# Optimization experiments

Measured on AMD Instinct MI355X. Metric: run time of the kernel, lower is better.

The kernel has to match this reference:

```python
import jax, jax.numpy as jnp
import numpy as np

HIDDEN_DIM = 512  # global scale divisor used in the original layer


def setup_inputs() -> dict:
    key = jax.random.key(0)
    k1, k2 = jax.random.split(key)
    B, S, H = 32, 8192, 512
    states_h = jax.random.normal(k1, (B, H), dtype=jnp.float32)
    enc_out = jax.random.normal(k2, (B, S, H), dtype=jnp.float32)
    return {"states_h": states_h, "enc_out": enc_out}


def reference(states_h, enc_out):
    # align_score = matmul(enc_out, dec_h^T) / hidden_dim -> [B, S, 1]
    align = jnp.einsum("bsh,bh->bs", enc_out, states_h) / HIDDEN_DIM
    # softmax over the sequence axis (axis=1 in the original [B,S,1] tensor)
    weights = jax.nn.softmax(align, axis=1)[:, :, None]           # [B, S, 1]
    # context = sum_s enc_out * weights -> [B, H], then expand to [B, 1, H]
    context = jnp.einsum("bsh,bs->bh", enc_out, weights[:, :, 0])
    context = context[:, None, :]                                  # [B, 1, H]
    return (context, weights)
```

## Files before the change

kernel.cpp:

```cpp
#include <hip/hip_runtime.h>
#include <hip/hip_bf16.h>
#include <math.h>


#define BB 32
#define SS 8192
#define HH 512
#define NB 32
#define WPB 4
#define NP (NB * WPB)
#define RPW (SS / NP)

__global__ __launch_bounds__(256, 4) void attn_pass1(
    const float* __restrict__ states, const float* __restrict__ enc,
    float* __restrict__ align, float* __restrict__ pm,
    float* __restrict__ pl, float* __restrict__ pC)
{
    const int b     = blockIdx.x >> 5;
    const int chunk = blockIdx.x & (NB - 1);
    const int lane  = threadIdx.x & 63;
    const int wv    = threadIdx.x >> 6;
    const int p     = chunk * WPB + wv;

    const float4* st = (const float4*)(states + (size_t)b * HH);
    const float4 sh0 = st[lane];
    const float4 sh1 = st[lane + 64];

    const float* rowbase = enc + ((size_t)b * SS + (size_t)p * RPW) * HH;

    float  m = -1e30f, l = 0.0f;
    float4 c0 = make_float4(0.f, 0.f, 0.f, 0.f);
    float4 c1 = make_float4(0.f, 0.f, 0.f, 0.f);
    float  my_a = 0.0f;

    #pragma unroll 4
    for (int r = 0; r < RPW; ++r) {
        const float4* rp = (const float4*)(rowbase + (size_t)r * HH);
        float4 e0 = rp[lane];
        float4 e1 = rp[lane + 64];

        float d = e0.x*sh0.x + e0.y*sh0.y + e0.z*sh0.z + e0.w*sh0.w
                + e1.x*sh1.x + e1.y*sh1.y + e1.z*sh1.z + e1.w*sh1.w;
        #pragma unroll
        for (int off = 1; off < 64; off <<= 1)
            d += __shfl_xor(d, off, 64);

        float a = d * (1.0f / 512.0f);
        my_a = (r == lane) ? a : my_a;

        float mn    = fmaxf(m, a);
        float scale = __expf(m - mn);
        float pr    = __expf(a - mn);
        l = fmaf(l, scale, pr);
        c0.x = fmaf(pr, e0.x, c0.x * scale);
        c0.y = fmaf(pr, e0.y, c0.y * scale);
        c0.z = fmaf(pr, e0.z, c0.z * scale);
        c0.w = fmaf(pr, e0.w, c0.w * scale);
        c1.x = fmaf(pr, e1.x, c1.x * scale);
        c1.y = fmaf(pr, e1.y, c1.y * scale);
        c1.z = fmaf(pr, e1.z, c1.z * scale);
        c1.w = fmaf(pr, e1.w, c1.w * scale);
        m = mn;
    }

    align[(size_t)b * SS + (size_t)p * RPW + lane] = my_a;
    if (lane == 0) {
        pm[b * NP + p] = m;
        pl[b * NP + p] = l;
    }
    float4* Cp = (float4*)(pC + (size_t)(b * NP + p) * HH);
    Cp[lane]      = c0;
    Cp[lane + 64] = c1;
}

__global__ __launch_bounds__(256) void attn_pass2(
    const float* __restrict__ align, const float* __restrict__ pm,
    const float* __restrict__ pl, const float* __restrict__ pC,
    float* __restrict__ out_ctx, float* __restrict__ out_w)
{
    const int b = blockIdx.x;
    const int t = threadIdx.x;

    __shared__ float red[NP];
    __shared__ float s_w[NP];
    __shared__ float s_M, s_invL;

    if (t < NP) red[t] = pm[b * NP + t];
    __syncthreads();
    if (t == 0) {
        float M = -1e30f;
        for (int i = 0; i < NP; ++i) M = fmaxf(M, red[i]);
        s_M = M;
    }
    __syncthreads();
    const float M = s_M;
    if (t < NP) s_w[t] = __expf(red[t] - M);
    __syncthreads();
    if (t == 0) {
        float L = 0.0f;
        for (int i = 0; i < NP; ++i) L += s_w[i] * pl[b * NP + i];
        s_invL = 1.0f / L;
    }
    __syncthreads();
    const float invL = s_invL;

    float acc0 = 0.0f, acc1 = 0.0f;
    const float* Cb = pC + (size_t)b * NP * HH;
    #pragma unroll 4
    for (int p = 0; p < NP; ++p) {
        float w = s_w[p];
        acc0 = fmaf(w, Cb[(size_t)p * HH + t], acc0);
        acc1 = fmaf(w, Cb[(size_t)p * HH + t + 256], acc1);
    }
    out_ctx[b * HH + t]       = acc0 * invL;
    out_ctx[b * HH + t + 256] = acc1 * invL;

    const float* al = align + (size_t)b * SS;
    float*       ow = out_w + (size_t)b * SS;
    for (int s = t; s < SS; s += 256)
        ow[s] = __expf(al[s] - M) * invL;
}

extern "C" void kernel_launch(void* const* d_in, const int* in_sizes, int n_in,
                              void* d_out, int out_size, void* d_ws, size_t ws_size,
                              hipStream_t stream) {
    const float* states = (const float*)d_in[0];
    const float* enc    = (const float*)d_in[1];

    float* out_ctx = (float*)d_out;
    float* out_w   = (float*)d_out + (size_t)BB * HH;

    float* ws_align = (float*)d_ws;
    float* ws_pm    = ws_align + (size_t)BB * SS;
    float* ws_pl    = ws_pm    + (size_t)BB * NP;
    float* ws_pC    = ws_pl    + (size_t)BB * NP;

    attn_pass1<<<BB * NB, 256, 0, stream>>>(states, enc, ws_align, ws_pm, ws_pl, ws_pC);
    attn_pass2<<<BB, 256, 0, stream>>>(ws_align, ws_pm, ws_pl, ws_pC, out_ctx, out_w);
}
```

Measured before the change: 684.4 us.

## Double the pass-1 split, prefetch rows, and parallelise pass-2 reduction across blocks

Pass 1 now uses 64 blocks per batch row, so each wave handles 32 rows instead of 64, and occupancy is raised to 6. Each wave software-prefetches encoder rows two iterations ahead. The online softmax update is made branchy on a wave-uniform score so that only one exp is computed per row. Pass 2 is split into 8 blocks per batch, with shuffle-based max/sum reductions, float4 accumulation of the partial contexts, and vectorised weight writes. The trade-off is doubling the partial-context workspace traffic and extra register pressure from the prefetch buffers.

```diff
diff --git a/kernel.cpp b/kernel.cpp
--- a/kernel.cpp
+++ b/kernel.cpp
@@ -6,17 +6,18 @@
 #define BB 32
 #define SS 8192
 #define HH 512
-#define NB 32
+#define NB 64
 #define WPB 4
 #define NP (NB * WPB)
 #define RPW (SS / NP)
+#define WCH 8
 
-__global__ __launch_bounds__(256, 4) void attn_pass1(
+__global__ __launch_bounds__(256, 6) void attn_pass1(
     const float* __restrict__ states, const float* __restrict__ enc,
     float* __restrict__ align, float* __restrict__ pm,
     float* __restrict__ pl, float* __restrict__ pC)
 {
-    const int b     = blockIdx.x >> 5;
+    const int b     = blockIdx.x >> 6;
     const int chunk = blockIdx.x & (NB - 1);
     const int lane  = threadIdx.x & 63;
     const int wv    = threadIdx.x >> 6;
@@ -26,18 +27,22 @@
     const float4 sh0 = st[lane];
     const float4 sh1 = st[lane + 64];
 
-    const float* rowbase = enc + ((size_t)b * SS + (size_t)p * RPW) * HH;
+    const float4* rp = (const float4*)(enc + ((size_t)b * SS + (size_t)p * RPW) * HH);
 
     float  m = -1e30f, l = 0.0f;
     float4 c0 = make_float4(0.f, 0.f, 0.f, 0.f);
     float4 c1 = make_float4(0.f, 0.f, 0.f, 0.f);
     float  my_a = 0.0f;
 
+    float4 e0 = rp[lane],        e1 = rp[lane + 64];
+    float4 f0 = rp[128 + lane],  f1 = rp[128 + lane + 64];
+
     #pragma unroll 4
     for (int r = 0; r < RPW; ++r) {
-        const float4* rp = (const float4*)(rowbase + (size_t)r * HH);
-        float4 e0 = rp[lane];
-        float4 e1 = rp[lane + 64];
+        const int rn = (r + 2 < RPW) ? (r + 2) : (RPW - 1);
+        const float4* q = rp + (size_t)rn * 128;
+        float4 g0 = q[lane];
+        float4 g1 = q[lane + 64];
 
         float d = e0.x*sh0.x + e0.y*sh0.y + e0.z*sh0.z + e0.w*sh0.w
                 + e1.x*sh1.x + e1.y*sh1.y + e1.z*sh1.z + e1.w*sh1.w;
@@ -46,24 +51,41 @@
             d += __shfl_xor(d, off, 64);
 
         float a = d * (1.0f / 512.0f);
+        a = __uint_as_float(__builtin_amdgcn_readfirstlane(__float_as_uint(a)));
+
         my_a = (r == lane) ? a : my_a;
 
-        float mn    = fmaxf(m, a);
-        float scale = __expf(m - mn);
-        float pr    = __expf(a - mn);
-        l = fmaf(l, scale, pr);
-        c0.x = fmaf(pr, e0.x, c0.x * scale);
-        c0.y = fmaf(pr, e0.y, c0.y * scale);
-        c0.z = fmaf(pr, e0.z, c0.z * scale);
-        c0.w = fmaf(pr, e0.w, c0.w * scale);
-        c1.x = fmaf(pr, e1.x, c1.x * scale);
-        c1.y = fmaf(pr, e1.y, c1.y * scale);
-        c1.z = fmaf(pr, e1.z, c1.z * scale);
-        c1.w = fmaf(pr, e1.w, c1.w * scale);
-        m = mn;
+        if (a > m) {
+            float sc = __expf(m - a);
+            l = fmaf(l, sc, 1.0f);
+            c0.x = fmaf(c0.x, sc, e0.x);
+            c0.y = fmaf(c0.y, sc, e0.y);
+            c0.z = fmaf(c0.z, sc, e0.z);
+            c0.w = fmaf(c0.w, sc, e0.w);
+            c1.x = fmaf(c1.x, sc, e1.x);
+            c1.y = fmaf(c1.y, sc, e1.y);
+            c1.z = fmaf(c1.z, sc, e1.z);
+            c1.w = fmaf(c1.w, sc, e1.w);
+            m = a;
+        } else {
+            float pr = __expf(a - m);
+            l += pr;
+            c0.x = fmaf(pr, e0.x, c0.x);
+            c0.y = fmaf(pr, e0.y, c0.y);
+            c0.z = fmaf(pr, e0.z, c0.z);
+            c0.w = fmaf(pr, e0.w, c0.w);
+            c1.x = fmaf(pr, e1.x, c1.x);
+            c1.y = fmaf(pr, e1.y, c1.y);
+            c1.z = fmaf(pr, e1.z, c1.z);
+            c1.w = fmaf(pr, e1.w, c1.w);
+        }
+
+        e0 = f0; e1 = f1;
+        f0 = g0; f1 = g1;
     }
 
-    align[(size_t)b * SS + (size_t)p * RPW + lane] = my_a;
+    if (lane < RPW)
+        align[(size_t)b * SS + (size_t)p * RPW + lane] = my_a;
     if (lane == 0) {
         pm[b * NP + p] = m;
         pl[b * NP + p] = l;
@@ -78,47 +100,81 @@
     const float* __restrict__ pl, const float* __restrict__ pC,
     float* __restrict__ out_ctx, float* __restrict__ out_w)
 {
-    const int b = blockIdx.x;
-    const int t = threadIdx.x;
+    const int b     = blockIdx.x >> 3;
+    const int chunk = blockIdx.x & (WCH - 1);
+    const int t     = threadIdx.x;
+    const int lane  = t & 63;
+    const int wv    = t >> 6;
 
-    __shared__ float red[NP];
-    __shared__ float s_w[NP];
-    __shared__ float s_M, s_invL;
+    __shared__ float  s_w[NP];
+    __shared__ float  s_red[8];
+    __shared__ float  s_bcast[2];
+    __shared__ float4 s_part[256];
 
-    if (t < NP) red[t] = pm[b * NP + t];
+    float pmv = pm[b * NP + t];
+    float plv = pl[b * NP + t];
+
+    float mx = pmv;
+    #pragma unroll
+    for (int off = 1; off < 64; off <<= 1)
+        mx = fmaxf(mx, __shfl_xor(mx, off, 64));
+    if (lane == 0) s_red[wv] = mx;
     __syncthreads();
-    if (t == 0) {
-        float M = -1e30f;
-        for (int i = 0; i < NP; ++i) M = fmaxf(M, red[i]);
-        s_M = M;
+    if (t == 0)
+        s_bcast[0] = fmaxf(fmaxf(s_red[0], s_red[1]), fmaxf(s_red[2], s_red[3]));
+    __syncthreads();
+    const float M = s_bcast[0];
+
+    float swv = __expf(pmv - M);
+    s_w[t] = swv;
+    float Lp = swv * plv;
+    #pragma unroll
+    for (int off = 1; off < 64; off <<= 1)
+        Lp += __shfl_xor(Lp, off, 64);
+    if (lane == 0) s_red[wv] = Lp;
+    __syncthreads();
+    if (t == 0)
+        s_bcast[1] = 1.0f / (s_red[0] + s_red[1] + s_red[2] + s_red[3]);
+    __syncthreads();
+    const float invL = s_bcast[1];
+
+    {
+        const int slot = t & 15;
+        const int pg   = t >> 4;
+        const float4* Cb4 = (const float4*)(pC + (size_t)b * NP * HH);
+        const int colbase = chunk * 16 + slot;
+        float4 acc = make_float4(0.f, 0.f, 0.f, 0.f);
+        #pragma unroll 4
+        for (int p = pg; p < NP; p += 16) {
+            float  w = s_w[p];
+            float4 v = Cb4[(size_t)p * 128 + colbase];
+            acc.x = fmaf(w, v.x, acc.x);
+            acc.y = fmaf(w, v.y, acc.y);
+            acc.z = fmaf(w, v.z, acc.z);
+            acc.w = fmaf(w, v.w, acc.w);
+        }
+        s_part[t] = acc;
+        __syncthreads();
+        if (t < 16) {
+            float4 tot = make_float4(0.f, 0.f, 0.f, 0.f);
+            #pragma unroll
+            for (int g = 0; g < 16; ++g) {
+                float4 v = s_part[g * 16 + t];
+                tot.x += v.x; tot.y += v.y; tot.z += v.z; tot.w += v.w;
+            }
+            float4* oc4 = (float4*)(out_ctx + (size_t)b * HH);
+            oc4[chunk * 16 + t] = make_float4(tot.x * invL, tot.y * invL,
+                                              tot.z * invL, tot.w * invL);
+        }
     }
-    __syncthreads();
-    const float M = s_M;
-    if (t < NP) s_w[t] = __expf(red[t] - M);
-    __syncthreads();
-    if (t == 0) {
-        float L = 0.0f;
-        for (int i = 0; i < NP; ++i) L += s_w[i] * pl[b * NP + i];
-        s_invL = 1.0f / L;
+
+    {
+        const float4* al4 = (const float4*)(align + (size_t)b * SS + chunk * 1024);
+        float4*       ow4 = (float4*)(out_w + (size_t)b * SS + chunk * 1024);
+        float4 v = al4[t];
+        ow4[t] = make_float4(__expf(v.x - M) * invL, __expf(v.y - M) * invL,
+                             __expf(v.z - M) * invL, __expf(v.w - M) * invL);
     }
-    __syncthreads();
-    const float invL = s_invL;
-
-    float acc0 = 0.0f, acc1 = 0.0f;
-    const float* Cb = pC + (size_t)b * NP * HH;
-    #pragma unroll 4
-    for (int p = 0; p < NP; ++p) {
-        float w = s_w[p];
-        acc0 = fmaf(w, Cb[(size_t)p * HH + t], acc0);
-        acc1 = fmaf(w, Cb[(size_t)p * HH + t + 256], acc1);
-    }
-    out_ctx[b * HH + t]       = acc0 * invL;
-    out_ctx[b * HH + t + 256] = acc1 * invL;
-
-    const float* al = align + (size_t)b * SS;
-    float*       ow = out_w + (size_t)b * SS;
-    for (int s = t; s < SS; s += 256)
-        ow[s] = __expf(al[s] - M) * invL;
 }
 
 extern "C" void kernel_launch(void* const* d_in, const int* in_sizes, int n_in,
@@ -136,5 +192,5 @@
     float* ws_pC    = ws_pl    + (size_t)BB * NP;
 
     attn_pass1<<<BB * NB, 256, 0, stream>>>(states, enc, ws_align, ws_pm, ws_pl, ws_pC);
-    attn_pass2<<<BB, 256, 0, stream>>>(ws_align, ws_pm, ws_pl, ws_pC, out_ctx, out_w);
+    attn_pass2<<<BB * WCH, 256, 0, stream>>>(ws_align, ws_pm, ws_pl, ws_pC, out_ctx, out_w);
 }
```

Result: no change. 687.2 us (+0.4%).
